# Performance work log

Measured on AMD Instinct MI355X. Metric: run time of the kernel, lower is better.

The kernel has to match this reference:

```python
import jax, jax.numpy as jnp
import numpy as np

N = 10000        # num_nodes
D = 256          # num_attrs
AVG_DEG = 32
K = N // 2       # known nodes
ALPHA = 0.5
BETA = 0.5


def setup_inputs() -> dict:
    rng = np.random.default_rng(0)
    # random graph -> symmetric adjacency (duplicate edges coalesce by summation,
    # matching torch_geometric coalescing of edge weights)
    src = rng.integers(0, N, size=N * AVG_DEG)
    dst = rng.integers(0, N, size=N * AVG_DEG)
    A = np.zeros((N, N), dtype=np.float32)
    np.add.at(A, (src, dst), 1.0)
    np.add.at(A, (dst, src), 1.0)
    # symmetric normalized Laplacian: L = I - D^{-1/2} A D^{-1/2}
    deg = A.sum(axis=1)
    dinv = np.where(deg > 0, 1.0 / np.sqrt(np.maximum(deg, 1e-12)), 0.0).astype(np.float32)
    L = np.eye(N, dtype=np.float32) - (dinv[:, None] * A * dinv[None, :])

    raw_x = rng.standard_normal((N, D)).astype(np.float32)
    know = np.sort(rng.choice(N, size=K, replace=False)).astype(np.int64)
    mean = raw_x[know].mean(axis=0)                 # is_binary=False path
    out_k_init = (raw_x[know] - mean).astype(np.float32)  # std = 1
    x = np.zeros((N, D), dtype=np.float32)
    x[know] = raw_x[know]                           # nn.Parameter init

    theta = np.float32((1.0 - 1.0 / N) * (1.0 / ALPHA - 1.0))
    eta = np.float32((1.0 / BETA - 1.0) / ALPHA)
    return {
        "x": jnp.asarray(x),
        "L": jnp.asarray(L),
        "mean": jnp.asarray(mean),
        "out_k_init": jnp.asarray(out_k_init),
        "know_mask": jnp.asarray(know),
        "theta": jnp.asarray(theta),
        "eta": jnp.asarray(eta),
    }


def reference(x, L, mean, out_k_init, know_mask, theta, eta):
    n = x.shape[0]
    xn = x - mean  # std = 1
    # dirichlet loss: sum_f x_f^T L x_f == sum(xn * (L @ xn))
    dirichlet = jnp.sum(xn * (L @ xn))
    # avg_L = n/(n-1) I - 1/(n-1) 11^T  ->  quadratic form in closed form
    col = xn.sum(axis=0)  # [D]
    avg = (n / (n - 1)) * jnp.sum(xn * xn) - (1.0 / (n - 1)) * jnp.sum(col * col)
    # MSE with reduction='sum'
    recon = jnp.sum((xn[know_mask] - out_k_init) ** 2)
    return -(dirichlet + eta * recon + theta * avg)
```

## Files before the change

kernel.cpp:

```cpp
#include <hip/hip_runtime.h>


#define NN    10000
#define DD    256
#define PREPB 157
#define SBLK  1250
#define QCAP  2048

typedef float  f32x4 __attribute__((ext_vector_type(4)));
typedef short  s16x8 __attribute__((ext_vector_type(8)));

__device__ __forceinline__ unsigned short f2bf(float f) {
    union { float f; unsigned u; } c; c.f = f;
    unsigned u = c.u;
    u += 0x7fffu + ((u >> 16) & 1u);
    return (unsigned short)(u >> 16);
}
__device__ __forceinline__ float bfr(unsigned short h) {
    union { unsigned u; float f; } c; c.u = ((unsigned)h) << 16; return c.f;
}

__global__ __launch_bounds__(256) void prep_kernel(const float* __restrict__ x,
                                                   const float* __restrict__ mean,
                                                   unsigned short* __restrict__ xnR,
                                                   float* __restrict__ csbuf,
                                                   float* __restrict__ ssbuf) {
    __shared__ __align__(16) unsigned short xs[64][264];
    __shared__ float red[4];
    const int t  = threadIdx.x;
    const int i0 = blockIdx.x * 64;
    const float mn = mean[t];
    float css = 0.f, ss = 0.f;
    for (int ii = 0; ii < 64; ++ii) {
        const int i = i0 + ii;
        float v = 0.f;
        if (i < NN) v = x[(size_t)i * DD + t] - mn;
        css += v; ss += v * v;
        xs[ii][t] = f2bf(v);
    }
    csbuf[(size_t)blockIdx.x * 256 + t] = css;
#pragma unroll
    for (int off = 32; off > 0; off >>= 1) ss += __shfl_xor(ss, off);
    if ((t & 63) == 0) red[t >> 6] = ss;
    __syncthreads();
    if (t == 0) ssbuf[blockIdx.x] = red[0] + red[1] + red[2] + red[3];
#pragma unroll
    for (int p = 0; p < 8; ++p) {
        const int row  = p * 8 + (t >> 5);
        const int colb = (t & 31) * 8;
        const int i = i0 + row;
        if (i < NN)
            *(s16x8*)(xnR + (size_t)i * DD + colb) = *(const s16x8*)&xs[row][colb];
    }
}

__global__ __launch_bounds__(256) void recon_kernel(const float* __restrict__ x,
                                                    const float* __restrict__ mean,
                                                    const float* __restrict__ oki,
                                                    const int* __restrict__ know,
                                                    int K, float* __restrict__ rbuf) {
    __shared__ float red[4];
    const int t = threadIdx.x;
    const float mn = mean[t];
    float s = 0.f;
    for (int b = blockIdx.x; b < K; b += gridDim.x) {
        const int idx = know[b];
        const float v = x[(size_t)idx * DD + t] - mn - oki[(size_t)b * DD + t];
        s += v * v;
    }
#pragma unroll
    for (int off = 32; off > 0; off >>= 1) s += __shfl_xor(s, off);
    if ((t & 63) == 0) red[t >> 6] = s;
    __syncthreads();
    if (t == 0) rbuf[blockIdx.x] = red[0] + red[1] + red[2] + red[3];
}

__global__ __launch_bounds__(256) void sdot_kernel(const float* __restrict__ L,
                                                   const unsigned short* __restrict__ xnR,
                                                   float* __restrict__ part) {
    __shared__ unsigned qidx[QCAP];
    __shared__ float    qval[QCAP];
    __shared__ unsigned qcnt;
    __shared__ float red[4];
    const int t = threadIdx.x;
    const int b = blockIdx.x;
    if (t == 0) qcnt = 0;
    __syncthreads();

    for (int rr = 0; rr < 8; ++rr) {
        const int i = (rr < 4) ? (4 * b + rr) : (NN - 8 - 4 * b + rr);
        const float* Lr = L + (size_t)i * NN;
        const int c0  = (i >> 2) << 2;
        const int nch = (NN - c0 + 7) >> 3;
        float cur[8];
        int m = t;
        if (m < nch) {
            const int c = c0 + (m << 3);
            if (c + 8 <= NN) {
                *(f32x4*)&cur[0] = *(const f32x4*)(Lr + c);
                *(f32x4*)&cur[4] = *(const f32x4*)(Lr + c + 4);
            } else {
#pragma unroll
                for (int e = 0; e < 8; ++e) cur[e] = (c + e < NN) ? Lr[c + e] : 0.f;
            }
        }
        while (m < nch) {
            const int m2 = m + 256;
            float nxt[8];
            if (m2 < nch) {
                const int c2 = c0 + (m2 << 3);
                if (c2 + 8 <= NN) {
                    *(f32x4*)&nxt[0] = *(const f32x4*)(Lr + c2);
                    *(f32x4*)&nxt[4] = *(const f32x4*)(Lr + c2 + 4);
                } else {
#pragma unroll
                    for (int e = 0; e < 8; ++e) nxt[e] = (c2 + e < NN) ? Lr[c2 + e] : 0.f;
                }
            }
            const int c = c0 + (m << 3);
#pragma unroll
            for (int e = 0; e < 8; ++e) {
                const float v = cur[e];
                const int j = c + e;
                if (v != 0.f && j >= i && j < NN) {
                    const float fv = (j == i) ? v : 2.f * v;
                    const unsigned slot = atomicAdd(&qcnt, 1u);
                    if (slot < QCAP) { qidx[slot] = ((unsigned)rr << 14) | (unsigned)j;
                                       qval[slot] = fv; }
                }
            }
#pragma unroll
            for (int e = 0; e < 8; ++e) cur[e] = nxt[e];
            m = m2;
        }
    }
    __syncthreads();
    const unsigned cnt = (qcnt < QCAP) ? qcnt : QCAP;

    const int grp = t >> 4;
    const int ln  = t & 15;
    float acc = 0.f;
    for (unsigned e = grp; e < cnt; e += 16) {
        const unsigned pk = qidx[e];
        const int rr = (int)(pk >> 14);
        const int j  = (int)(pk & 16383u);
        const int i  = (rr < 4) ? (4 * b + rr) : (NN - 8 - 4 * b + rr);
        const unsigned short* ri = xnR + (size_t)i * DD + ln * 16;
        const unsigned short* rj = xnR + (size_t)j * DD + ln * 16;
        const s16x8 a0 = *(const s16x8*)ri, a1 = *(const s16x8*)(ri + 8);
        const s16x8 b0 = *(const s16x8*)rj, b1 = *(const s16x8*)(rj + 8);
        float d = 0.f;
#pragma unroll
        for (int k = 0; k < 8; ++k) d += bfr((unsigned short)a0[k]) * bfr((unsigned short)b0[k]);
#pragma unroll
        for (int k = 0; k < 8; ++k) d += bfr((unsigned short)a1[k]) * bfr((unsigned short)b1[k]);
#pragma unroll
        for (int off = 1; off < 16; off <<= 1) d += __shfl_xor(d, off);
        if (ln == 0) acc += qval[e] * d;
    }
#pragma unroll
    for (int off = 32; off > 0; off >>= 1) acc += __shfl_xor(acc, off);
    if ((t & 63) == 0) red[t >> 6] = acc;
    __syncthreads();
    if (t == 0) part[b] = red[0] + red[1] + red[2] + red[3];
}

__global__ __launch_bounds__(256) void fin_kernel(const float* __restrict__ part,
                                                  const float* __restrict__ csbuf,
                                                  const float* __restrict__ ssbuf,
                                                  const float* __restrict__ rbuf,
                                                  const float* __restrict__ theta,
                                                  const float* __restrict__ eta,
                                                  float* __restrict__ out) {
    __shared__ float red[4][4];
    const int t = threadIdx.x;
    float sp = 0.f;
    for (int i = t; i < SBLK; i += 256) sp += part[i];
    float cs = 0.f;
    for (int bb = 0; bb < PREPB; ++bb) cs += csbuf[(size_t)bb * 256 + t];
    float c2 = cs * cs;
    float ssv = (t < PREPB) ? ssbuf[t] : 0.f;
    float rv  = rbuf[t];
#pragma unroll
    for (int off = 32; off > 0; off >>= 1) {
        sp  += __shfl_xor(sp, off);
        c2  += __shfl_xor(c2, off);
        ssv += __shfl_xor(ssv, off);
        rv  += __shfl_xor(rv, off);
    }
    if ((t & 63) == 0) {
        red[t >> 6][0] = sp; red[t >> 6][1] = c2;
        red[t >> 6][2] = ssv; red[t >> 6][3] = rv;
    }
    __syncthreads();
    if (t == 0) {
        float dir = 0.f, colsq = 0.f, ss = 0.f, rec = 0.f;
#pragma unroll
        for (int w = 0; w < 4; ++w) {
            dir += red[w][0]; colsq += red[w][1];
            ss  += red[w][2]; rec   += red[w][3];
        }
        const float n = (float)NN;
        const float avg = (n / (n - 1.f)) * ss - colsq / (n - 1.f);
        out[0] = -(dir + eta[0] * rec + theta[0] * avg);
    }
}

extern "C" void kernel_launch(void* const* d_in, const int* in_sizes, int n_in,
                              void* d_out, int out_size, void* d_ws, size_t ws_size,
                              hipStream_t stream) {
    const float* x     = (const float*)d_in[0];
    const float* L     = (const float*)d_in[1];
    const float* mean  = (const float*)d_in[2];
    const float* oki   = (const float*)d_in[3];
    const int*   know  = (const int*)d_in[4];
    const float* theta = (const float*)d_in[5];
    const float* eta   = (const float*)d_in[6];
    float* out = (float*)d_out;

    char* ws = (char*)d_ws;
    unsigned short* xnR = (unsigned short*)ws;
    float* part  = (float*)(ws + 6 * 1024 * 1024);
    float* csbuf = (float*)(ws + 7 * 1024 * 1024);
    float* ssbuf = (float*)(ws + 8 * 1024 * 1024);
    float* rbuf  = (float*)(ws + 8 * 1024 * 1024 + 4096);
    const int K = in_sizes[4];

    hipLaunchKernelGGL(prep_kernel,  dim3(PREPB), dim3(256), 0, stream, x, mean, xnR, csbuf, ssbuf);
    hipLaunchKernelGGL(recon_kernel, dim3(256),   dim3(256), 0, stream, x, mean, oki, know, K, rbuf);
    hipLaunchKernelGGL(sdot_kernel,  dim3(SBLK),  dim3(256), 0, stream, L, xnR, part);
    hipLaunchKernelGGL(fin_kernel,   dim3(1),     dim3(256), 0, stream, part, csbuf, ssbuf, rbuf, theta, eta, out);
}
```

Measured before the change: 101.6 us.

## Flatten row scan into triple-buffered 16-wide chunks and pair gather dot products

The per-row scan of the dense Laplacian is flattened into a single chunk index space covering all 8 rows a block handles. Each thread now loads 16 floats per chunk and keeps three chunks in flight, so there is no per-row loop boundary and more memory loads are outstanding. The gather phase computes two sparse-entry dot products per iteration to raise memory-level parallelism. This costs more registers and prefix-sum decode arithmetic per chunk, which may lower occupancy.

```diff
diff --git a/kernel.cpp b/kernel.cpp
--- a/kernel.cpp
+++ b/kernel.cpp
@@ -87,76 +87,121 @@
     if (t == 0) qcnt = 0;
     __syncthreads();
 
-    for (int rr = 0; rr < 8; ++rr) {
-        const int i = (rr < 4) ? (4 * b + rr) : (NN - 8 - 4 * b + rr);
-        const float* Lr = L + (size_t)i * NN;
-        const int c0  = (i >> 2) << 2;
-        const int nch = (NN - c0 + 7) >> 3;
-        float cur[8];
-        int m = t;
-        if (m < nch) {
-            const int c = c0 + (m << 3);
-            if (c + 8 <= NN) {
-                *(f32x4*)&cur[0] = *(const f32x4*)(Lr + c);
-                *(f32x4*)&cur[4] = *(const f32x4*)(Lr + c + 4);
-            } else {
-#pragma unroll
-                for (int e = 0; e < 8; ++e) cur[e] = (c + e < NN) ? Lr[c + e] : 0.f;
-            }
-        }
-        while (m < nch) {
-            const int m2 = m + 256;
-            float nxt[8];
-            if (m2 < nch) {
-                const int c2 = c0 + (m2 << 3);
-                if (c2 + 8 <= NN) {
-                    *(f32x4*)&nxt[0] = *(const f32x4*)(Lr + c2);
-                    *(f32x4*)&nxt[4] = *(const f32x4*)(Lr + c2 + 4);
-                } else {
-#pragma unroll
-                    for (int e = 0; e < 8; ++e) nxt[e] = (c2 + e < NN) ? Lr[c2 + e] : 0.f;
-                }
-            }
-            const int c = c0 + (m << 3);
-#pragma unroll
-            for (int e = 0; e < 8; ++e) {
-                const float v = cur[e];
-                const int j = c + e;
-                if (v != 0.f && j >= i && j < NN) {
-                    const float fv = (j == i) ? v : 2.f * v;
-                    const unsigned slot = atomicAdd(&qcnt, 1u);
-                    if (slot < QCAP) { qidx[slot] = ((unsigned)rr << 14) | (unsigned)j;
-                                       qval[slot] = fv; }
-                }
-            }
-#pragma unroll
-            for (int e = 0; e < 8; ++e) cur[e] = nxt[e];
-            m = m2;
-        }
-    }
+    const int ibt = 4 * b;
+    const int ibb = NN - 8 - 4 * b;
+#define ROWLEN(i_) ((NN - (((i_) >> 2) << 2) + 15) >> 4)
+    const int l0 = ROWLEN(ibt);     const int l1 = ROWLEN(ibt + 1);
+    const int l2 = ROWLEN(ibt + 2); const int l3 = ROWLEN(ibt + 3);
+    const int l4 = ROWLEN(ibb + 4); const int l5 = ROWLEN(ibb + 5);
+    const int l6 = ROWLEN(ibb + 6);
+    const int pre1 = l0;        const int pre2 = pre1 + l1;
+    const int pre3 = pre2 + l2; const int pre4 = pre3 + l3;
+    const int pre5 = pre4 + l4; const int pre6 = pre5 + l5;
+    const int pre7 = pre6 + l6;
+    const int ntot = pre7 + ROWLEN(ibb + 7);
+#undef ROWLEN
+
+#define DECODE(g_)                                                             \
+    int rr_ = 0, base_ = 0;                                                    \
+    if ((g_) >= pre1) { rr_ = 1; base_ = pre1; }                               \
+    if ((g_) >= pre2) { rr_ = 2; base_ = pre2; }                               \
+    if ((g_) >= pre3) { rr_ = 3; base_ = pre3; }                               \
+    if ((g_) >= pre4) { rr_ = 4; base_ = pre4; }                               \
+    if ((g_) >= pre5) { rr_ = 5; base_ = pre5; }                               \
+    if ((g_) >= pre6) { rr_ = 6; base_ = pre6; }                               \
+    if ((g_) >= pre7) { rr_ = 7; base_ = pre7; }                               \
+    const int i_ = (rr_ < 4) ? (ibt + rr_) : (ibb + rr_);                      \
+    const int c_ = (((i_) >> 2) << 2) + (((g_) - base_) << 4);
+
+#define ISSUE(V0_, V1_, V2_, V3_, g_) {                                        \
+    if ((g_) < ntot) {                                                         \
+        DECODE(g_)                                                             \
+        const float* p_ = L + (size_t)i_ * NN + c_;                            \
+        if (c_ + 16 <= NN) {                                                   \
+            V0_ = *(const f32x4*)p_;        V1_ = *(const f32x4*)(p_ + 4);     \
+            V2_ = *(const f32x4*)(p_ + 8);  V3_ = *(const f32x4*)(p_ + 12);    \
+        } else {                                                               \
+            _Pragma("unroll") for (int e_ = 0; e_ < 4; ++e_) {                 \
+                V0_[e_] = (c_ + e_      < NN) ? p_[e_]      : 0.f;             \
+                V1_[e_] = (c_ + e_ + 4  < NN) ? p_[e_ + 4]  : 0.f;             \
+                V2_[e_] = (c_ + e_ + 8  < NN) ? p_[e_ + 8]  : 0.f;             \
+                V3_[e_] = (c_ + e_ + 12 < NN) ? p_[e_ + 12] : 0.f;             \
+            } } } }
+
+#define PROC(V0_, V1_, V2_, V3_, g_) {                                         \
+    if ((g_) < ntot) {                                                         \
+        DECODE(g_)                                                             \
+        _Pragma("unroll") for (int e_ = 0; e_ < 16; ++e_) {                    \
+            const float v_ = (e_ < 4) ? V0_[e_] : (e_ < 8) ? V1_[e_ - 4]       \
+                           : (e_ < 12) ? V2_[e_ - 8] : V3_[e_ - 12];           \
+            const int j_ = c_ + e_;                                            \
+            if (v_ != 0.f && j_ >= i_ && j_ < NN) {                            \
+                const unsigned s_ = atomicAdd(&qcnt, 1u);                      \
+                if (s_ < QCAP) {                                               \
+                    qidx[s_] = ((unsigned)rr_ << 14) | (unsigned)j_;           \
+                    qval[s_] = (j_ == i_) ? v_ : 2.f * v_;                     \
+                } } } } }
+
+    f32x4 A0, A1, A2, A3, B0, B1, B2, B3, C0, C1, C2, C3;
+    int g = t;
+    ISSUE(A0, A1, A2, A3, g)
+    ISSUE(B0, B1, B2, B3, g + 256)
+    ISSUE(C0, C1, C2, C3, g + 512)
+    while (g < ntot) {
+        PROC (A0, A1, A2, A3, g)
+        ISSUE(A0, A1, A2, A3, g + 768)
+        PROC (B0, B1, B2, B3, g + 256)
+        ISSUE(B0, B1, B2, B3, g + 1024)
+        PROC (C0, C1, C2, C3, g + 512)
+        ISSUE(C0, C1, C2, C3, g + 1280)
+        g += 768;
+    }
+#undef ISSUE
+#undef PROC
+#undef DECODE
     __syncthreads();
     const unsigned cnt = (qcnt < QCAP) ? qcnt : QCAP;
 
     const int grp = t >> 4;
     const int ln  = t & 15;
     float acc = 0.f;
-    for (unsigned e = grp; e < cnt; e += 16) {
-        const unsigned pk = qidx[e];
-        const int rr = (int)(pk >> 14);
-        const int j  = (int)(pk & 16383u);
-        const int i  = (rr < 4) ? (4 * b + rr) : (NN - 8 - 4 * b + rr);
-        const unsigned short* ri = xnR + (size_t)i * DD + ln * 16;
-        const unsigned short* rj = xnR + (size_t)j * DD + ln * 16;
-        const s16x8 a0 = *(const s16x8*)ri, a1 = *(const s16x8*)(ri + 8);
-        const s16x8 b0 = *(const s16x8*)rj, b1 = *(const s16x8*)(rj + 8);
-        float d = 0.f;
-#pragma unroll
-        for (int k = 0; k < 8; ++k) d += bfr((unsigned short)a0[k]) * bfr((unsigned short)b0[k]);
-#pragma unroll
-        for (int k = 0; k < 8; ++k) d += bfr((unsigned short)a1[k]) * bfr((unsigned short)b1[k]);
-#pragma unroll
-        for (int off = 1; off < 16; off <<= 1) d += __shfl_xor(d, off);
-        if (ln == 0) acc += qval[e] * d;
+    for (unsigned e = grp; e < cnt; e += 32) {
+        const unsigned e2   = e + 16;
+        const bool     has2 = (e2 < cnt);
+        const unsigned pkA = qidx[e];
+        const unsigned pkB = has2 ? qidx[e2] : pkA;
+        const int rrA = (int)(pkA >> 14), jA = (int)(pkA & 16383u);
+        const int rrB = (int)(pkB >> 14), jB = (int)(pkB & 16383u);
+        const int iA  = (rrA < 4) ? (ibt + rrA) : (ibb + rrA);
+        const int iB  = (rrB < 4) ? (ibt + rrB) : (ibb + rrB);
+        const unsigned short* riA = xnR + (size_t)iA * DD + ln * 16;
+        const unsigned short* rjA = xnR + (size_t)jA * DD + ln * 16;
+        const unsigned short* riB = xnR + (size_t)iB * DD + ln * 16;
+        const unsigned short* rjB = xnR + (size_t)jB * DD + ln * 16;
+        const s16x8 a0 = *(const s16x8*)riA, a1 = *(const s16x8*)(riA + 8);
+        const s16x8 b0 = *(const s16x8*)rjA, b1 = *(const s16x8*)(rjA + 8);
+        const s16x8 c0 = *(const s16x8*)riB, c1 = *(const s16x8*)(riB + 8);
+        const s16x8 d0 = *(const s16x8*)rjB, d1 = *(const s16x8*)(rjB + 8);
+        float dA = 0.f, dB = 0.f;
+#pragma unroll
+        for (int k = 0; k < 8; ++k) {
+            dA += bfr((unsigned short)a0[k]) * bfr((unsigned short)b0[k]);
+            dB += bfr((unsigned short)c0[k]) * bfr((unsigned short)d0[k]);
+        }
+#pragma unroll
+        for (int k = 0; k < 8; ++k) {
+            dA += bfr((unsigned short)a1[k]) * bfr((unsigned short)b1[k]);
+            dB += bfr((unsigned short)c1[k]) * bfr((unsigned short)d1[k]);
+        }
+#pragma unroll
+        for (int off = 1; off < 16; off <<= 1) {
+            dA += __shfl_xor(dA, off);
+            dB += __shfl_xor(dB, off);
+        }
+        if (ln == 0) {
+            acc += qval[e] * dA;
+            if (has2) acc += qval[e2] * dB;
+        }
     }
 #pragma unroll
     for (int off = 32; off > 0; off >>= 1) acc += __shfl_xor(acc, off);
```

Result: no change. 101.8 us (+0.2%).
